# Kernel tuning notes

Hardware: AMD Instinct MI355X
Metric: run time of the kernel (lower is better)

Reference implementation:

```python
import jax, jax.numpy as jnp
import numpy as np

D_MODEL = 1024
NUM_HEADS = 16
D_KEY = D_MODEL // NUM_HEADS


def setup_inputs() -> dict:
    key = jax.random.key(0)
    ks = jax.random.split(key, 9)
    B, S = 2, 2048
    s = 1.0 / np.sqrt(D_MODEL)
    return {
        "x": jax.random.normal(ks[0], (B, S, D_MODEL), dtype=jnp.float32),
        "W_q": jax.random.normal(ks[1], (D_MODEL, D_MODEL), dtype=jnp.float32) * s,
        "b_q": jnp.zeros((D_MODEL,), dtype=jnp.float32),
        "W_k": jax.random.normal(ks[2], (D_MODEL, D_MODEL), dtype=jnp.float32) * s,
        "b_k": jnp.zeros((D_MODEL,), dtype=jnp.float32),
        "W_v": jax.random.normal(ks[3], (D_MODEL, D_MODEL), dtype=jnp.float32) * s,
        "b_v": jnp.zeros((D_MODEL,), dtype=jnp.float32),
        "W_o": jax.random.normal(ks[4], (D_MODEL, D_MODEL), dtype=jnp.float32) * s,
        "b_o": jnp.zeros((D_MODEL,), dtype=jnp.float32),
    }


def reference(x, W_q, b_q, W_k, b_k, W_v, b_v, W_o, b_o):
    B, S, _ = x.shape
    # Linear projections (torch nn.Linear: x @ W.T + b; here W stored as [in, out])
    Q = x @ W_q + b_q
    K = x @ W_k + b_k
    V = x @ W_v + b_v
    # [B, S, H, dk] -> [B, H, S, dk]
    def split_heads(t):
        return t.reshape(B, S, NUM_HEADS, D_KEY).transpose(0, 2, 1, 3)
    Q, K, V = split_heads(Q), split_heads(K), split_heads(V)
    scale = 1.0 / np.sqrt(D_KEY).astype(np.float32)
    logits = jnp.einsum("bhqd,bhkd->bhqk", Q, K) * scale  # [B,H,S,S]
    weights = jax.nn.softmax(logits, axis=-1)
    ctx = jnp.einsum("bhqk,bhkd->bhqd", weights, V)       # [B,H,S,dk]
    concat = ctx.transpose(0, 2, 1, 3).reshape(B, S, D_MODEL)
    return concat @ W_o + b_o
```

## Files before the change

kernel.cpp:

```cpp
#include <hip/hip_runtime.h>
#include <cstdint>
#include <cstddef>

#define SEQ   2048
#define NH    16
#define DK    64
#define DM    1024
#define MTOT  4096
#define QSCALE (0.125f * 1.44269504088896f)

typedef __attribute__((ext_vector_type(8))) short           short8;
typedef __attribute__((ext_vector_type(8))) unsigned short  ushort8;
typedef __attribute__((ext_vector_type(4))) unsigned short  ushort4v;
typedef __attribute__((ext_vector_type(2))) unsigned int    uint2v;
typedef __attribute__((ext_vector_type(4))) unsigned int    uint4v;
typedef __attribute__((ext_vector_type(4))) float           float4v;
typedef unsigned short u16;
typedef unsigned int   u32;

__device__ inline float4v mfma16(short8 a, short8 b, float4v c) {
    return __builtin_amdgcn_mfma_f32_16x16x32_bf16(a, b, c, 0, 0, 0);
}
__device__ inline u16 f2bf(float f) {
    u32 u = __float_as_uint(f);
    u += 0x7fffu + ((u >> 16) & 1u);
    return (u16)(u >> 16);
}
__device__ inline u32 pkbf(float a, float b) {
    u32 r;
    asm("v_cvt_pk_bf16_f32 %0, %1, %2" : "=v"(r) : "v"(a), "v"(b));
    return r;
}
__device__ inline float ex2(float x) {
    float r;
    asm("v_exp_f32 %0, %1" : "=v"(r) : "v"(x));
    return r;
}
__device__ inline void pl32swap(u32& a, u32& b) {
    asm("v_permlane32_swap_b32 %0, %1" : "+v"(a), "+v"(b));
}
__device__ inline void pl16swap(u32& a, u32& b) {
    asm("v_permlane16_swap_b32 %0, %1" : "+v"(a), "+v"(b));
}
__device__ inline void gld16(const void* g, void* lds) {
    __builtin_amdgcn_global_load_lds(
        (const __attribute__((address_space(1))) u32*)g,
        (__attribute__((address_space(3))) u32*)lds, 16, 0, 0);
}

__global__ __launch_bounds__(256)
void convert_x(const float* __restrict__ x, u16* __restrict__ xb)
{
    const int i = blockIdx.x * 256 + threadIdx.x;
    const float4v a = ((const float4v*)x)[2 * i];
    const float4v b = ((const float4v*)x)[2 * i + 1];
    ushort8 o;
    #pragma unroll
    for (int j = 0; j < 4; j++) { o[j] = f2bf(a[j]); o[4 + j] = f2bf(b[j]); }
    ((ushort8*)xb)[i] = o;
}

__global__ __launch_bounds__(256)
void transpose_w(const float* __restrict__ W0, const float* __restrict__ W1,
                 const float* __restrict__ W2, const float* __restrict__ W3,
                 u16* __restrict__ T0, u16* __restrict__ T1,
                 u16* __restrict__ T2, u16* __restrict__ T3)
{
    __shared__ u16 t[64][68];
    const float* W; u16* T;
    switch (blockIdx.z) {
        case 0: W = W0; T = T0; break;
        case 1: W = W1; T = T1; break;
        case 2: W = W2; T = T2; break;
        default: W = W3; T = T3; break;
    }
    const int n0 = blockIdx.x * 64, k0 = blockIdx.y * 64;
    const int r  = threadIdx.x >> 4;
    const int c4 = (threadIdx.x & 15) * 4;
    #pragma unroll
    for (int i = 0; i < 4; i++) {
        float4v v = *(const float4v*)&W[(size_t)(k0 + r + i * 16) * DM + n0 + c4];
        #pragma unroll
        for (int j = 0; j < 4; j++) t[r + i * 16][c4 + j] = f2bf(v[j]);
    }
    __syncthreads();
    #pragma unroll
    for (int i = 0; i < 4; i++) {
        const int rr = r + i * 16;
        ushort4v o;
        #pragma unroll
        for (int j = 0; j < 4; j++) o[j] = t[c4 + j][rr];
        *(ushort4v*)&T[(size_t)(n0 + rr) * DM + k0 + c4] = o;
    }
}

template<int TM, int MODE>
__global__ __launch_bounds__(512)
void gemm_bt(const u16* __restrict__ A, const u16* __restrict__ WT,
             const float* __restrict__ bq, const float* __restrict__ bk,
             const float* __restrict__ bv,
             void* __restrict__ out0, u16* __restrict__ outK, u16* __restrict__ outV)
{
    constexpr int NT = 512;
    constexpr int MF = TM / 32;
    __shared__ u16 Al[TM][64];
    __shared__ u16 Bl[128][64];
    const int tid  = threadIdx.x;
    const int lane = tid & 63, w = tid >> 6;
    const int quad = lane >> 4, l16 = lane & 15;

    const int nxb  = gridDim.x;
    const int wgid = blockIdx.y * nxb + blockIdx.x;
    const int per  = (nxb * gridDim.y) >> 3;
    const int nl   = (wgid & 7) * per + (wgid >> 3);
    const int n0 = (nl % nxb) * 128, m0 = (nl / nxb) * TM;

    const int wm = (w >> 2) * (TM / 2);
    const int wn = (w & 3) * 32;

    float4v acc[MF][2] = {};

    for (int k0 = 0; k0 < DM; k0 += 64) {
        __syncthreads();
        #pragma unroll
        for (int j = 0; j < TM * 8 / NT; j++) {
            const int c = j * NT + tid;
            const int row = c >> 3, kc = c & 7;
            gld16(A + (size_t)(m0 + row) * DM + k0 + ((kc ^ (row & 7)) * 8),
                  &Al[0][0] + (size_t)(j * NT + w * 64) * 8);
        }
        #pragma unroll
        for (int j = 0; j < 1024 / NT; j++) {
            const int c = j * NT + tid;
            const int row = c >> 3, kc = c & 7;
            gld16(WT + (size_t)(n0 + row) * DM + k0 + ((kc ^ (row & 7)) * 8),
                  &Bl[0][0] + (size_t)(j * NT + w * 64) * 8);
        }
        __syncthreads();
        #pragma unroll
        for (int u = 0; u < 2; u++) {
            short8 af[MF], bf[2];
            #pragma unroll
            for (int mi = 0; mi < MF; mi++) {
                const int row = wm + mi * 16 + l16;
                af[mi] = *(const short8*)&Al[row][((4 * u + quad) ^ (row & 7)) * 8];
            }
            #pragma unroll
            for (int ni = 0; ni < 2; ni++) {
                const int row = wn + ni * 16 + l16;
                bf[ni] = *(const short8*)&Bl[row][((4 * u + quad) ^ (row & 7)) * 8];
            }
            #pragma unroll
            for (int mi = 0; mi < MF; mi++)
                #pragma unroll
                for (int ni = 0; ni < 2; ni++)
                    acc[mi][ni] = mfma16(af[mi], bf[ni], acc[mi][ni]);
        }
    }

    if constexpr (MODE == 0) {
        float* out = (float*)out0;
        #pragma unroll
        for (int ni = 0; ni < 2; ni++) {
            const int col = n0 + wn + ni * 16 + l16;
            const float bb = bq[col];
            #pragma unroll
            for (int mi = 0; mi < MF; mi++)
                #pragma unroll
                for (int r = 0; r < 4; r++) {
                    const int row = m0 + wm + mi * 16 + quad * 4 + r;
                    out[(size_t)row * DM + col] = acc[mi][ni][r] + bb;
                }
        }
    } else {
        const int seg = n0 >> 10;
        u16* outp = (seg == 0) ? (u16*)out0 : (seg == 1 ? outK : outV);
        const float* bias = (seg == 0) ? bq : (seg == 1 ? bk : bv);
        const float scl = (seg == 0) ? QSCALE : 1.0f;
        if (seg < 2) {
            #pragma unroll
            for (int ni = 0; ni < 2; ni++) {
                const int col = (n0 & 1023) + wn + ni * 16 + l16;
                const float bb = bias[col];
                const int h = col >> 6, d = col & 63;
                #pragma unroll
                for (int mi = 0; mi < MF; mi++)
                    #pragma unroll
                    for (int r = 0; r < 4; r++) {
                        const int row = m0 + wm + mi * 16 + quad * 4 + r;
                        const int b = row >> 11, s = row & (SEQ - 1);
                        outp[(((size_t)(b * NH + h) * SEQ + s) << 6) + d] =
                            f2bf((acc[mi][ni][r] + bb) * scl);
                    }
            }
        } else {
            #pragma unroll
            for (int ni = 0; ni < 2; ni++) {
                const int col = (n0 & 1023) + wn + ni * 16 + l16;
                const float bb = bias[col];
                const int h = col >> 6, d = col & 63;
                #pragma unroll
                for (int mi = 0; mi < MF; mi++) {
                    const int row0 = m0 + wm + mi * 16 + quad * 4;
                    const int b = row0 >> 11, s = row0 & (SEQ - 1);
                    uint2v pv;
                    pv[0] = pkbf(acc[mi][ni][0] + bb, acc[mi][ni][1] + bb);
                    pv[1] = pkbf(acc[mi][ni][2] + bb, acc[mi][ni][3] + bb);
                    *(uint2v*)&outp[(((size_t)((b * NH + h) * DK + d)) << 11) + s] = pv;
                }
            }
        }
    }
}

__global__ __launch_bounds__(512, 4)
void attn_kernel(const u16* __restrict__ Q, const u16* __restrict__ K,
                 const u16* __restrict__ VT, u16* __restrict__ Ctx)
{
    __shared__ u16 Kl[2][2][32][64];
    __shared__ u16 Vl[2][2][64][32];
    __shared__ float Xl[4][64][17];

    const int tid  = threadIdx.x;
    const int lane = tid & 63, w = tid >> 6;
    const int wq = w & 3, wgrp = w >> 2;
    const int quad = lane >> 4, l16 = lane & 15;

    const int wgid = blockIdx.y * 16 + blockIdx.x;
    const int nlin = (wgid & 7) * 64 + (wgid >> 3);
    const int qt = nlin & 15;
    const int bh = nlin >> 4;
    const size_t head = (size_t)bh * SEQ * DK;

    short8 qf[2][2];
    #pragma unroll
    for (int g = 0; g < 2; g++) {
        const size_t qrow = head + (size_t)(qt * 128 + wq * 32 + g * 16 + l16) * DK;
        qf[g][0] = *(const short8*)(Q + qrow + quad * 8);
        qf[g][1] = *(const short8*)(Q + qrow + 32 + quad * 8);
    }

    float4v acc[2][4] = {};
    float l_part[2] = {0.f, 0.f};

    const int sh = tid >> 8;
    const int rK = (tid >> 3) & 31, cK = tid & 7;
    const int dV = (tid >> 2) & 63, cV = tid & 3;
    const int sVk = (dV & 3) ^ ((dV >> 2) & 3);
    const u16* const Kg = K  + head + (size_t)(sh * 1024 + rK) * DK + (cK ^ (rK & 7)) * 8;
    const u16* const Vg = VT + head + (size_t)dV * SEQ + sh * 1024 + (cV ^ sVk) * 8;
    u16* const Kdst = &Kl[0][0][0][0] + tid * 8;
    u16* const Vdst = &Vl[0][0][0][0] + tid * 8;

    gld16(Kg, Kdst);
    gld16(Vg, Vdst);

    for (int it = 0; it < 32; it++) {
        const int cur = it & 1;
        __syncthreads();
        if (it + 1 < 32) {
            gld16(Kg + (size_t)(it + 1) * 32 * DK, Kdst + (cur ^ 1) * 4096);
            gld16(Vg + (size_t)(it + 1) * 32,      Vdst + (cur ^ 1) * 4096);
        }

        short8 kf[2][2];
        #pragma unroll
        for (int t = 0; t < 2; t++) {
            const int row = t * 16 + l16;
            kf[t][0] = *(const short8*)&Kl[cur][wgrp][row][(quad ^ (row & 7)) * 8];
            kf[t][1] = *(const short8*)&Kl[cur][wgrp][row][((4 + quad) ^ (row & 7)) * 8];
        }
        float4v z[2][2];
        __builtin_amdgcn_s_setprio(1);
        #pragma unroll
        for (int t = 0; t < 2; t++)
            #pragma unroll
            for (int g = 0; g < 2; g++) {
                float4v zz = {};
                zz = mfma16(kf[t][0], qf[g][0], zz);
                zz = mfma16(kf[t][1], qf[g][1], zz);
                z[t][g] = zz;
            }
        __builtin_amdgcn_s_setprio(0);

        short8 pf[2];
        #pragma unroll
        for (int g = 0; g < 2; g++) {
            float p[2][4];
            #pragma unroll
            for (int t = 0; t < 2; t++) {
                p[t][0] = ex2(z[t][g][0]); p[t][1] = ex2(z[t][g][1]);
                p[t][2] = ex2(z[t][g][2]); p[t][3] = ex2(z[t][g][3]);
                l_part[g] += (p[t][0] + p[t][1]) + (p[t][2] + p[t][3]);
            }
            u32 A = pkbf(p[0][0], p[0][1]);
            u32 B = pkbf(p[0][2], p[0][3]);
            u32 C = pkbf(p[1][0], p[1][1]);
            u32 D = pkbf(p[1][2], p[1][3]);
            pl32swap(A, C); pl16swap(A, C);
            pl32swap(B, D); pl16swap(B, D);
            uint4v pw; pw[0] = A; pw[1] = B; pw[2] = C; pw[3] = D;
            pf[g] = __builtin_bit_cast(short8, pw);
        }

        __builtin_amdgcn_s_setprio(1);
        #pragma unroll
        for (int t = 0; t < 4; t++) {
            const int d = t * 16 + l16;
            const short8 vf =
                *(const short8*)&Vl[cur][wgrp][d][(quad ^ ((d & 3) ^ ((d >> 2) & 3))) * 8];
            acc[0][t] = mfma16(vf, pf[0], acc[0][t]);
            acc[1][t] = mfma16(vf, pf[1], acc[1][t]);
        }
        __builtin_amdgcn_s_setprio(0);
    }

    #pragma unroll
    for (int g = 0; g < 2; g++) {
        l_part[g] += __shfl_xor(l_part[g], 16);
        l_part[g] += __shfl_xor(l_part[g], 32);
    }

    float ltot[2];
    #pragma unroll
    for (int p = 0; p < 2; p++) {
        __syncthreads();
        if (wgrp == 1) {
            #pragma unroll
            for (int g = 0; g < 2; g++)
                #pragma unroll
                for (int tt = 0; tt < 2; tt++)
                    #pragma unroll
                    for (int r = 0; r < 4; r++)
                        Xl[wq][lane][g * 8 + tt * 4 + r] = acc[g][2 * p + tt][r];
            Xl[wq][lane][16] = l_part[p];
        }
        __syncthreads();
        if (wgrp == 0) {
            #pragma unroll
            for (int g = 0; g < 2; g++)
                #pragma unroll
                for (int tt = 0; tt < 2; tt++)
                    #pragma unroll
                    for (int r = 0; r < 4; r++)
                        acc[g][2 * p + tt][r] += Xl[wq][lane][g * 8 + tt * 4 + r];
            ltot[p] = l_part[p] + Xl[wq][lane][16];
        }
    }

    if (wgrp == 0) {
        const int b = bh >> 4, h = bh & 15;
        #pragma unroll
        for (int g = 0; g < 2; g++) {
            const float rl = 1.0f / ltot[g];
            const int s = qt * 128 + wq * 32 + g * 16 + l16;
            u16* dst = Ctx + (size_t)(b * SEQ + s) * DM + h * 64 + quad * 4;
            #pragma unroll
            for (int t = 0; t < 4; t++) {
                uint2v ov;
                ov[0] = pkbf(acc[g][t][0] * rl, acc[g][t][1] * rl);
                ov[1] = pkbf(acc[g][t][2] * rl, acc[g][t][3] * rl);
                *(uint2v*)&dst[t * 16] = ov;
            }
        }
    }
}

extern "C" void kernel_launch(void* const* d_in, const int* in_sizes, int n_in,
                              void* d_out, int out_size, void* d_ws, size_t ws_size,
                              hipStream_t stream)
{
    const float* x   = (const float*)d_in[0];
    const float* W_q = (const float*)d_in[1];
    const float* b_q = (const float*)d_in[2];
    const float* W_k = (const float*)d_in[3];
    const float* b_k = (const float*)d_in[4];
    const float* W_v = (const float*)d_in[5];
    const float* b_v = (const float*)d_in[6];
    const float* W_o = (const float*)d_in[7];
    const float* b_o = (const float*)d_in[8];

    u16* xb  = (u16*)d_ws;
    u16* WT  = xb + (size_t)MTOT * DM;
    u16* WTo = WT + (size_t)3 * DM * DM;
    u16* VTb = WTo + (size_t)DM * DM;
    u16* Cb  = xb;
    u16* Qb  = (u16*)d_out;
    u16* Kb  = Qb + (size_t)MTOT * DM;

    convert_x<<<2048, 256, 0, stream>>>(x, xb);
    transpose_w<<<dim3(16, 16, 4), 256, 0, stream>>>(
        W_q, W_k, W_v, W_o, WT, WT + (size_t)DM * DM, WT + (size_t)2 * DM * DM, WTo);
    gemm_bt<128, 1><<<dim3(24, 32), 512, 0, stream>>>(xb, WT, b_q, b_k, b_v, Qb, Kb, VTb);
    attn_kernel<<<dim3(SEQ / 128, 2 * NH), 512, 0, stream>>>(Qb, Kb, VTb, Cb);
    gemm_bt<64, 0><<<dim3(8, 64), 512, 0, stream>>>(Cb, WTo, b_o, nullptr, nullptr,
                                                    (float*)d_out, nullptr, nullptr);
}
```

Measured before the change: 186.9 us.

## Software-pipeline attention loop: overlap QK of next tile with softmax/PV

Restructures the attention inner loop so the QK^T MFMAs for tile it run alongside the exp/pack and PV MFMAs for tile it-1. The K/V LDS staging grows from a double buffer to a 4-deep ring with prefetch distance 2, and the cross-wave reduction scratch now reuses the same pool. The aim is to hide the dependency between QK results and the exp/pack work, and to give loads more lead time. The catch is that LDS per block rises to 64KB and register pressure goes up from keeping the previous tile's logits live, which may cut the number of resident blocks.

```diff
diff --git a/kernel.cpp b/kernel.cpp
--- a/kernel.cpp
+++ b/kernel.cpp
@@ -217,9 +217,7 @@
 void attn_kernel(const u16* __restrict__ Q, const u16* __restrict__ K,
                  const u16* __restrict__ VT, u16* __restrict__ Ctx)
 {
-    __shared__ u16 Kl[2][2][32][64];
-    __shared__ u16 Vl[2][2][64][32];
-    __shared__ float Xl[4][64][17];
+    __shared__ __align__(16) u16 pool[32768];
 
     const int tid  = threadIdx.x;
     const int lane = tid & 63, w = tid >> 6;
@@ -249,28 +247,18 @@
     const int sVk = (dV & 3) ^ ((dV >> 2) & 3);
     const u16* const Kg = K  + head + (size_t)(sh * 1024 + rK) * DK + (cK ^ (rK & 7)) * 8;
     const u16* const Vg = VT + head + (size_t)dV * SEQ + sh * 1024 + (cV ^ sVk) * 8;
-    u16* const Kdst = &Kl[0][0][0][0] + tid * 8;
-    u16* const Vdst = &Vl[0][0][0][0] + tid * 8;
-
-    gld16(Kg, Kdst);
-    gld16(Vg, Vdst);
-
-    for (int it = 0; it < 32; it++) {
-        const int cur = it & 1;
-        __syncthreads();
-        if (it + 1 < 32) {
-            gld16(Kg + (size_t)(it + 1) * 32 * DK, Kdst + (cur ^ 1) * 4096);
-            gld16(Vg + (size_t)(it + 1) * 32,      Vdst + (cur ^ 1) * 4096);
-        }
-
+    u16* const Kdst = pool + tid * 8;
+    u16* const Vdst = pool + 16384 + tid * 8;
+
+    auto QKSTEP = [&](int cur, float4v znew[2][2]) {
         short8 kf[2][2];
         #pragma unroll
         for (int t = 0; t < 2; t++) {
             const int row = t * 16 + l16;
-            kf[t][0] = *(const short8*)&Kl[cur][wgrp][row][(quad ^ (row & 7)) * 8];
-            kf[t][1] = *(const short8*)&Kl[cur][wgrp][row][((4 + quad) ^ (row & 7)) * 8];
-        }
-        float4v z[2][2];
+            const u16* kb = pool + cur * 4096 + wgrp * 2048 + row * 64;
+            kf[t][0] = *(const short8*)(kb + (quad ^ (row & 7)) * 8);
+            kf[t][1] = *(const short8*)(kb + ((4 + quad) ^ (row & 7)) * 8);
+        }
         __builtin_amdgcn_s_setprio(1);
         #pragma unroll
         for (int t = 0; t < 2; t++)
@@ -279,18 +267,19 @@
                 float4v zz = {};
                 zz = mfma16(kf[t][0], qf[g][0], zz);
                 zz = mfma16(kf[t][1], qf[g][1], zz);
-                z[t][g] = zz;
+                znew[t][g] = zz;
             }
         __builtin_amdgcn_s_setprio(0);
-
-        short8 pf[2];
+    };
+
+    auto SMPACK = [&](float4v zp[2][2], short8 pf[2]) {
         #pragma unroll
         for (int g = 0; g < 2; g++) {
             float p[2][4];
             #pragma unroll
             for (int t = 0; t < 2; t++) {
-                p[t][0] = ex2(z[t][g][0]); p[t][1] = ex2(z[t][g][1]);
-                p[t][2] = ex2(z[t][g][2]); p[t][3] = ex2(z[t][g][3]);
+                p[t][0] = ex2(zp[t][g][0]); p[t][1] = ex2(zp[t][g][1]);
+                p[t][2] = ex2(zp[t][g][2]); p[t][3] = ex2(zp[t][g][3]);
                 l_part[g] += (p[t][0] + p[t][1]) + (p[t][2] + p[t][3]);
             }
             u32 A = pkbf(p[0][0], p[0][1]);
@@ -302,17 +291,55 @@
             uint4v pw; pw[0] = A; pw[1] = B; pw[2] = C; pw[3] = D;
             pf[g] = __builtin_bit_cast(short8, pw);
         }
-
+    };
+
+    auto PVSTEP = [&](int pv, short8 pf[2]) {
         __builtin_amdgcn_s_setprio(1);
         #pragma unroll
         for (int t = 0; t < 4; t++) {
             const int d = t * 16 + l16;
+            const u16* vb = pool + 16384 + pv * 4096 + wgrp * 2048 + d * 32;
             const short8 vf =
-                *(const short8*)&Vl[cur][wgrp][d][(quad ^ ((d & 3) ^ ((d >> 2) & 3))) * 8];
+                *(const short8*)(vb + (quad ^ ((d & 3) ^ ((d >> 2) & 3))) * 8);
             acc[0][t] = mfma16(vf, pf[0], acc[0][t]);
             acc[1][t] = mfma16(vf, pf[1], acc[1][t]);
         }
         __builtin_amdgcn_s_setprio(0);
+    };
+
+    gld16(Kg,                 Kdst);
+    gld16(Vg,                 Vdst);
+    gld16(Kg + 32 * DK,       Kdst + 4096);
+    gld16(Vg + 32,            Vdst + 4096);
+
+    float4v zp[2][2];
+
+    __syncthreads();
+    gld16(Kg + (size_t)2 * 32 * DK, Kdst + 2 * 4096);
+    gld16(Vg + (size_t)2 * 32,      Vdst + 2 * 4096);
+    QKSTEP(0, zp);
+
+    for (int it = 1; it < 32; ++it) {
+        const int cur = it & 3, pv = (it - 1) & 3;
+        __syncthreads();
+        if (it + 2 < 32) {
+            gld16(Kg + (size_t)(it + 2) * 32 * DK, Kdst + ((it + 2) & 3) * 4096);
+            gld16(Vg + (size_t)(it + 2) * 32,      Vdst + ((it + 2) & 3) * 4096);
+        }
+        float4v zn[2][2];
+        QKSTEP(cur, zn);
+        short8 pf[2];
+        SMPACK(zp, pf);
+        PVSTEP(pv, pf);
+        #pragma unroll
+        for (int t = 0; t < 2; t++)
+            #pragma unroll
+            for (int g = 0; g < 2; g++) zp[t][g] = zn[t][g];
+    }
+    {
+        short8 pf[2];
+        SMPACK(zp, pf);
+        PVSTEP(3, pf);
     }
 
     #pragma unroll
@@ -321,6 +348,8 @@
         l_part[g] += __shfl_xor(l_part[g], 32);
     }
 
+    float* const Xlp = (float*)pool;
+    #define XL(a, b, c) Xlp[(((a) * 64 + (b)) * 17) + (c)]
     float ltot[2];
     #pragma unroll
     for (int p = 0; p < 2; p++) {
@@ -332,8 +361,8 @@
                 for (int tt = 0; tt < 2; tt++)
                     #pragma unroll
                     for (int r = 0; r < 4; r++)
-                        Xl[wq][lane][g * 8 + tt * 4 + r] = acc[g][2 * p + tt][r];
-            Xl[wq][lane][16] = l_part[p];
+                        XL(wq, lane, g * 8 + tt * 4 + r) = acc[g][2 * p + tt][r];
+            XL(wq, lane, 16) = l_part[p];
         }
         __syncthreads();
         if (wgrp == 0) {
@@ -343,10 +372,11 @@
                 for (int tt = 0; tt < 2; tt++)
                     #pragma unroll
                     for (int r = 0; r < 4; r++)
-                        acc[g][2 * p + tt][r] += Xl[wq][lane][g * 8 + tt * 4 + r];
-            ltot[p] = l_part[p] + Xl[wq][lane][16];
-        }
-    }
+                        acc[g][2 * p + tt][r] += XL(wq, lane, g * 8 + tt * 4 + r);
+            ltot[p] = l_part[p] + XL(wq, lane, 16);
+        }
+    }
+    #undef XL
 
     if (wgrp == 0) {
         const int b = bh >> 4, h = bh & 15;
```

Result: no change. 185.1 us (-1.0%).
